# Kernel tuning notes

Measured on AMD Instinct MI355X. Metric: run time of the kernel, lower is better.

## Reference

```python
import jax, jax.numpy as jnp
import numpy as np

BATCH, CLASSES = 32768, 1000
SMOOTHING = 0.1  # timm-style LabelSmoothingCrossEntropy default


def setup_inputs() -> dict:
    key = jax.random.key(0)
    k1, k2 = jax.random.split(key)
    output = jax.random.normal(k1, (BATCH, CLASSES), dtype=jnp.float32)
    target = jax.random.randint(k2, (BATCH,), 0, CLASSES, dtype=jnp.int64)
    return {"output": output, "target": target}


def _label_smoothing_ce(x, target, smoothing=SMOOTHING):
    # timm-style: loss = (1-eps)*NLL + eps*mean(-logp)
    logp = jax.nn.log_softmax(x, axis=-1)
    nll = -jnp.take_along_axis(logp, target[:, None], axis=-1)[:, 0]
    smooth = -logp.mean(axis=-1)
    return ((1.0 - smoothing) * nll + smoothing * smooth).mean()


def reference(output, target):
    batch, classes = output.shape
    probs = jax.nn.softmax(output, axis=1)  # [B, C]
    # per-class empirical frequency via one-pass bincount
    counts = jnp.zeros((classes,), dtype=probs.dtype).at[target].add(1.0)
    avg_count = counts / batch                 # [C]
    avg_conf = probs.mean(axis=0)              # [C]
    loss_mdca = jnp.abs(avg_conf - avg_count).sum() / classes
    # faithful to original: label-smoothing CE applied to softmaxed output
    loss_ce = _label_smoothing_ce(probs, target)
    loss = loss_ce + loss_mdca
    return (loss, loss_ce, loss_mdca)
```

## Files before the change

### kernel.cpp

```cpp
#include <hip/hip_runtime.h>
#include <math.h>

#define BATCH   32768
#define CLASSES 1000
#define C4      (CLASSES / 4)
#define EPS     0.1f
#define LOG1001 6.9087547794f

#define MB   512
#define MT   512
#define WPB  8
#define NPROC (MB * WPB)
#define RPW   (BATCH / NPROC)

#define PSTRIDE   2048
#define PARTIAL_F 0
#define STAGE2_F  (MB * PSTRIDE)
#define SCAL_F    (STAGE2_F + 8 * PSTRIDE)

__global__ __launch_bounds__(MT)
void mdca_main(const float* __restrict__ x, const int* __restrict__ target,
               float* __restrict__ partial, float* __restrict__ scal) {
    __shared__ float cs[WPB][1024];
    __shared__ float cnt[1024];
    __shared__ float red[2][WPB];

    const int tid  = threadIdx.x;
    const int wave = tid >> 6;
    const int lane = tid & 63;

    float4* my4 = reinterpret_cast<float4*>(cs[wave]);
    #pragma unroll
    for (int k = 0; k < 4; ++k) my4[64 * k + lane] = make_float4(0.f, 0.f, 0.f, 0.f);
    cnt[tid] = 0.f; cnt[tid + 512] = 0.f;
    __syncthreads();

    const int proc = blockIdx.x * WPB + wave;
    const int r0   = proc * RPW;

    int t[RPW];
    #pragma unroll
    for (int s = 0; s < RPW; ++s) t[s] = target[r0 + s];

    const float4* base4 = reinterpret_cast<const float4*>(x + (size_t)r0 * CLASSES);
    float4 v[RPW][4];
    #pragma unroll
    for (int s = 0; s < RPW; ++s) {
        #pragma unroll
        for (int k = 0; k < 4; ++k) {
            const int idx4 = 64 * k + lane;
            v[s][k] = (idx4 < C4) ? base4[s * C4 + idx4]
                                  : make_float4(-INFINITY, -INFINITY, -INFINITY, -INFINITY);
        }
    }

    float z[RPW], et[RPW];
    #pragma unroll
    for (int s = 0; s < RPW; ++s) {
        float zl = 0.f, el = 0.f;
        #pragma unroll
        for (int k = 0; k < 4; ++k) {
            float4 e;
            e.x = __expf(v[s][k].x); e.y = __expf(v[s][k].y);
            e.z = __expf(v[s][k].z); e.w = __expf(v[s][k].w);
            v[s][k] = e;
            zl += (e.x + e.y) + (e.z + e.w);
            const int d = t[s] - 4 * (64 * k + lane);
            if ((unsigned)d < 4u)
                el = (d == 0) ? e.x : (d == 1) ? e.y : (d == 2) ? e.z : e.w;
        }
        z[s] = zl; et[s] = el;
    }
    #pragma unroll
    for (int o = 32; o > 0; o >>= 1) {
        #pragma unroll
        for (int s = 0; s < RPW; ++s) z[s] += __shfl_xor(z[s], o, 64);
    }

    float iz[RPW];
    float q = 0.f, pa = 0.f;
    #pragma unroll
    for (int s = 0; s < RPW; ++s) {
        iz[s] = 1.0f / z[s];
        pa   += et[s] * iz[s];
    }

    #pragma unroll
    for (int k = 0; k < 4; ++k) {
        const int idx4 = 64 * k + lane;
        if (idx4 < C4) {
            float4 col = my4[idx4];
            #pragma unroll
            for (int s = 0; s < RPW; ++s) {
                const float px = v[s][k].x * iz[s]; col.x += px; q = fmaf(px, px, q);
                const float py = v[s][k].y * iz[s]; col.y += py; q = fmaf(py, py, q);
                const float pz = v[s][k].z * iz[s]; col.z += pz; q = fmaf(pz, pz, q);
                const float pw = v[s][k].w * iz[s]; col.w += pw; q = fmaf(pw, pw, q);
            }
            my4[idx4] = col;
        }
    }

    if (lane == 0) {
        #pragma unroll
        for (int s = 0; s < RPW; ++s) atomicAdd(&cnt[t[s]], 1.0f);
    }

    #pragma unroll
    for (int o = 32; o > 0; o >>= 1) {
        q  += __shfl_xor(q,  o, 64);
        pa += __shfl_xor(pa, o, 64);
    }
    if (lane == 0) { red[0][wave] = q; red[1][wave] = pa; }
    __syncthreads();

    float* ps = partial + (size_t)blockIdx.x * PSTRIDE;
    for (int c = tid; c < 1024; c += MT) {
        float s = 0.f;
        #pragma unroll
        for (int w = 0; w < WPB; ++w) s += cs[w][c];
        ps[c]        = s;
        ps[1024 + c] = cnt[c];
    }
    if (tid == 0) {
        float sq = 0.f, sp = 0.f;
        for (int w = 0; w < WPB; ++w) { sq += red[0][w]; sp += red[1][w]; }
        atomicAdd(&scal[0], sq);
        atomicAdd(&scal[1], sp);
    }
}

__global__ __launch_bounds__(128)
void mdca_reduce(const float* __restrict__ partial, float* __restrict__ stage2) {
    const int bg = blockIdx.x >> 4;
    const int cg = blockIdx.x & 15;
    const int cc = cg * 128 + threadIdx.x;
    const int b0 = bg * (MB / 8);
    float acc = 0.f;
    for (int b = b0; b < b0 + MB / 8; ++b)
        acc += partial[(size_t)b * PSTRIDE + cc];
    stage2[(size_t)bg * PSTRIDE + cc] = acc;
}

__global__ __launch_bounds__(1024)
void mdca_final(const float* __restrict__ stage2, const float* __restrict__ scal,
                float* __restrict__ out) {
    __shared__ float red[16];
    const int tid = threadIdx.x, wave = tid >> 6, lane = tid & 63;
    float d = 0.f;
    if (tid < CLASSES) {
        float conf = 0.f, c2 = 0.f;
        #pragma unroll
        for (int bg = 0; bg < 8; ++bg) {
            conf += stage2[bg * PSTRIDE + tid];
            c2   += stage2[bg * PSTRIDE + 1024 + tid];
        }
        d = fabsf(conf - c2) * (1.0f / BATCH);
    }
    #pragma unroll
    for (int o = 32; o > 0; o >>= 1) d += __shfl_xor(d, o, 64);
    if (lane == 0) red[wave] = d;
    __syncthreads();
    if (tid == 0) {
        float tot = 0.f;
        for (int w = 0; w < 16; ++w) tot += red[w];
        const float mdca = tot / CLASSES;
        const float ce = LOG1001 + 0.5f * scal[0] / (1001.0f * BATCH)
                       - (1.0f - EPS) * (scal[1] * (1.0f / BATCH))
                       - EPS / CLASSES;
        out[0] = ce + mdca;
        out[1] = ce;
        out[2] = mdca;
    }
}

extern "C" void kernel_launch(void* const* d_in, const int* in_sizes, int n_in,
                              void* d_out, int out_size, void* d_ws, size_t ws_size,
                              hipStream_t stream) {
    const float* x   = (const float*)d_in[0];
    const int*   tgt = (const int*)d_in[1];
    float* out = (float*)d_out;
    float* ws  = (float*)d_ws;

    hipMemsetAsync(ws + SCAL_F, 0, 2 * sizeof(float), stream);

    mdca_main<<<MB, MT, 0, stream>>>(x, tgt, ws + PARTIAL_F, ws + SCAL_F);
    mdca_reduce<<<128, 128, 0, stream>>>(ws + PARTIAL_F, ws + STAGE2_F);
    mdca_final<<<1, 1024, 0, stream>>>(ws + STAGE2_F, ws + SCAL_F, out);
}
```

Baseline: 202.6 us.

## Use more smaller blocks, drop global atomics and memset, fold scalars into partials

Moves the main kernel from 512 blocks of 8 waves to 2048 blocks of 4 waves, adds a launch-bounds occupancy hint, and cuts rows per wave from 8 to 4, which lowers register pressure and spreads work more evenly. The two global scalar atomics and the memset launch are removed: per-block scalar sums now go into unused slots 1000/1001 of the partial buffer and are reduced through the existing two-stage path. The reduce kernel gets four independent accumulators for more memory-level parallelism. The cost is a 4x larger partial buffer that the reduce stage must read, 256 rows serially per thread.

```diff
diff --git a/kernel.cpp b/kernel.cpp
--- a/kernel.cpp
+++ b/kernel.cpp
@@ -7,20 +7,19 @@
 #define EPS     0.1f
 #define LOG1001 6.9087547794f
 
-#define MB   512
-#define MT   512
-#define WPB  8
+#define MB   2048
+#define MT   256
+#define WPB  4
 #define NPROC (MB * WPB)
 #define RPW   (BATCH / NPROC)
 
 #define PSTRIDE   2048
 #define PARTIAL_F 0
 #define STAGE2_F  (MB * PSTRIDE)
-#define SCAL_F    (STAGE2_F + 8 * PSTRIDE)
-
-__global__ __launch_bounds__(MT)
+
+__global__ __launch_bounds__(MT, 4)
 void mdca_main(const float* __restrict__ x, const int* __restrict__ target,
-               float* __restrict__ partial, float* __restrict__ scal) {
+               float* __restrict__ partial) {
     __shared__ float cs[WPB][1024];
     __shared__ float cnt[1024];
     __shared__ float red[2][WPB];
@@ -32,7 +31,8 @@
     float4* my4 = reinterpret_cast<float4*>(cs[wave]);
     #pragma unroll
     for (int k = 0; k < 4; ++k) my4[64 * k + lane] = make_float4(0.f, 0.f, 0.f, 0.f);
-    cnt[tid] = 0.f; cnt[tid + 512] = 0.f;
+    #pragma unroll
+    for (int c = tid; c < 1024; c += MT) cnt[c] = 0.f;
     __syncthreads();
 
     const int proc = blockIdx.x * WPB + wave;
@@ -115,18 +115,22 @@
     __syncthreads();
 
     float* ps = partial + (size_t)blockIdx.x * PSTRIDE;
+    #pragma unroll
     for (int c = tid; c < 1024; c += MT) {
-        float s = 0.f;
-        #pragma unroll
-        for (int w = 0; w < WPB; ++w) s += cs[w][c];
-        ps[c]        = s;
+        if (c < 1000) {
+            float s = 0.f;
+            #pragma unroll
+            for (int w = 0; w < WPB; ++w) s += cs[w][c];
+            ps[c] = s;
+        }
         ps[1024 + c] = cnt[c];
     }
     if (tid == 0) {
         float sq = 0.f, sp = 0.f;
+        #pragma unroll
         for (int w = 0; w < WPB; ++w) { sq += red[0][w]; sp += red[1][w]; }
-        atomicAdd(&scal[0], sq);
-        atomicAdd(&scal[1], sp);
+        ps[1000] = sq;
+        ps[1001] = sp;
     }
 }
 
@@ -136,15 +140,18 @@
     const int cg = blockIdx.x & 15;
     const int cc = cg * 128 + threadIdx.x;
     const int b0 = bg * (MB / 8);
-    float acc = 0.f;
-    for (int b = b0; b < b0 + MB / 8; ++b)
-        acc += partial[(size_t)b * PSTRIDE + cc];
-    stage2[(size_t)bg * PSTRIDE + cc] = acc;
+    float a0 = 0.f, a1 = 0.f, a2 = 0.f, a3 = 0.f;
+    for (int b = b0; b < b0 + MB / 8; b += 4) {
+        a0 += partial[(size_t)(b + 0) * PSTRIDE + cc];
+        a1 += partial[(size_t)(b + 1) * PSTRIDE + cc];
+        a2 += partial[(size_t)(b + 2) * PSTRIDE + cc];
+        a3 += partial[(size_t)(b + 3) * PSTRIDE + cc];
+    }
+    stage2[(size_t)bg * PSTRIDE + cc] = (a0 + a1) + (a2 + a3);
 }
 
 __global__ __launch_bounds__(1024)
-void mdca_final(const float* __restrict__ stage2, const float* __restrict__ scal,
-                float* __restrict__ out) {
+void mdca_final(const float* __restrict__ stage2, float* __restrict__ out) {
     __shared__ float red[16];
     const int tid = threadIdx.x, wave = tid >> 6, lane = tid & 63;
     float d = 0.f;
@@ -163,10 +170,17 @@
     __syncthreads();
     if (tid == 0) {
         float tot = 0.f;
+        #pragma unroll
         for (int w = 0; w < 16; ++w) tot += red[w];
+        float q = 0.f, pa = 0.f;
+        #pragma unroll
+        for (int bg = 0; bg < 8; ++bg) {
+            q  += stage2[bg * PSTRIDE + 1000];
+            pa += stage2[bg * PSTRIDE + 1001];
+        }
         const float mdca = tot / CLASSES;
-        const float ce = LOG1001 + 0.5f * scal[0] / (1001.0f * BATCH)
-                       - (1.0f - EPS) * (scal[1] * (1.0f / BATCH))
+        const float ce = LOG1001 + 0.5f * q / (1001.0f * BATCH)
+                       - (1.0f - EPS) * (pa * (1.0f / BATCH))
                        - EPS / CLASSES;
         out[0] = ce + mdca;
         out[1] = ce;
@@ -182,9 +196,7 @@
     float* out = (float*)d_out;
     float* ws  = (float*)d_ws;
 
-    hipMemsetAsync(ws + SCAL_F, 0, 2 * sizeof(float), stream);
-
-    mdca_main<<<MB, MT, 0, stream>>>(x, tgt, ws + PARTIAL_F, ws + SCAL_F);
+    mdca_main<<<MB, MT, 0, stream>>>(x, tgt, ws + PARTIAL_F);
     mdca_reduce<<<128, 128, 0, stream>>>(ws + PARTIAL_F, ws + STAGE2_F);
-    mdca_final<<<1, 1024, 0, stream>>>(ws + STAGE2_F, ws + SCAL_F, out);
-}
+    mdca_final<<<1, 1024, 0, stream>>>(ws + STAGE2_F, out);
+}
```

New measurement: 218.8 us. 8.0% more time.
